# Performance work log

Hardware: AMD Instinct MI355X
Metric: run time of the kernel (lower is better)

The kernel has to match this reference:

```python
import jax, jax.numpy as jnp
import numpy as np

N = 200000
E = 3200000
EPS = 1e-5


def setup_inputs() -> dict:
    key = jax.random.key(0)
    ks = jax.random.split(key, 8)
    x = jax.random.normal(ks[0], (N, 128), dtype=jnp.float32)
    edge_index = jax.random.randint(ks[1], (2, E), 0, N, dtype=jnp.int32)
    def lin(k, fi, fo):
        s = 1.0 / np.sqrt(fi)
        return jax.random.uniform(k, (fi, fo), jnp.float32, -s, s)
    return {
        "x": x,
        "edge_index": edge_index,
        "W1": lin(ks[2], 128, 256), "b1": jnp.zeros((256,), jnp.float32),
        "gamma1": jnp.ones((256,), jnp.float32), "beta1": jnp.zeros((256,), jnp.float32),
        "W2": lin(ks[3], 256, 256), "b2": jnp.zeros((256,), jnp.float32),
        "gamma2": jnp.ones((256,), jnp.float32), "beta2": jnp.zeros((256,), jnp.float32),
        "W3": lin(ks[4], 256, 40), "b3": jnp.zeros((40,), jnp.float32),
    }


def _gcn_norm(edge_index):
    # add self-loops, compute symmetric GCN normalization
    loop = jnp.arange(N, dtype=jnp.int32)
    row = jnp.concatenate([edge_index[0], loop])
    col = jnp.concatenate([edge_index[1], loop])
    deg = jax.ops.segment_sum(jnp.ones_like(row, dtype=jnp.float32), row, num_segments=N)
    dinv = jax.lax.rsqrt(jnp.maximum(deg, 1.0))  # deg >= 1 due to self-loops
    norm = dinv[row] * dinv[col]  # [E+N]
    return row, col, norm


def _gcn_conv(x, W, b, row, col, norm):
    h = x @ W                                  # [N, Fout] small GEMM
    msg = h[col] * norm[:, None]               # gather + scale  [E+N, Fout]
    out = jax.ops.segment_sum(msg, row, num_segments=N)  # scatter-add
    return out + b


def _batchnorm(x, gamma, beta):
    mu = jnp.mean(x, axis=0)
    var = jnp.var(x, axis=0)
    return (x - mu) * jax.lax.rsqrt(var + EPS) * gamma + beta


def reference(x, edge_index, W1, b1, gamma1, beta1, W2, b2, gamma2, beta2, W3, b3):
    row, col, norm = _gcn_norm(edge_index)
    h = _gcn_conv(x, W1, b1, row, col, norm)
    h = jax.nn.relu(_batchnorm(h, gamma1, beta1))
    h = _gcn_conv(h, W2, b2, row, col, norm)
    h = jax.nn.relu(_batchnorm(h, gamma2, beta2))
    h = _gcn_conv(h, W3, b3, row, col, norm)
    return jax.nn.log_softmax(h, axis=-1)
```

## Files before the change

### kernel.cpp

```cpp
#include <hip/hip_runtime.h>
#include <hip/hip_bf16.h>

#define NNODES 200000
#define NEDGES 3200000
#define NBUCK 782
#define NEB 512
#define EPB (NEDGES / NEB)
#define EPS 1e-5f
#define AGGB_CHUNK 50000

typedef __bf16 bf16x8 __attribute__((ext_vector_type(8)));
typedef float  f32x4  __attribute__((ext_vector_type(4)));
typedef float  f32x2  __attribute__((ext_vector_type(2)));

__device__ __forceinline__ float bflo(unsigned u) { return __uint_as_float(u << 16); }
__device__ __forceinline__ float bfhi(unsigned u) { return __uint_as_float(u & 0xffff0000u); }
__device__ __forceinline__ unsigned short f2b(float f) {
    return __builtin_bit_cast(unsigned short, __float2bfloat16(f));
}
__device__ __forceinline__ unsigned pk2(float a, float b) {
    return (unsigned)f2b(a) | ((unsigned)f2b(b) << 16);
}
__device__ __forceinline__ unsigned bnrelu_pk(unsigned u, f32x2 c, f32x2 h) {
    f32x2 v = { __uint_as_float(u << 16), __uint_as_float(u & 0xffff0000u) };
    v = __builtin_elementwise_fma(v, c, h);
    const f32x2 z = {0.f, 0.f};
    v = __builtin_elementwise_max(v, z);
    return pk2(v[0], v[1]);
}

__device__ __forceinline__ void prepw_one(const float* __restrict__ W,
                                          unsigned short* __restrict__ Wswz,
                                          int K, int NOUT, int t) {
    int KSTEPS = K / 32;
    int lane = t & 63;
    int ks = (t >> 6) % KSTEPS;
    int g  = (t >> 6) / KSTEPS;
    int c = lane & 15, q = lane >> 4;
    int col = g * 16 + c;
    int k0 = ks * 32 + q * 8;
    unsigned short vals[8];
#pragma unroll
    for (int j = 0; j < 8; ++j)
        vals[j] = (col < NOUT) ? f2b(W[(size_t)(k0 + j) * NOUT + col]) : (unsigned short)0;
    *(uint4*)((char*)Wswz + (size_t)t * 16) = __builtin_bit_cast(uint4, vals);
}

__global__ __launch_bounds__(256) void k_cnt(const int* __restrict__ row, int* __restrict__ cnt,
                                             const float* __restrict__ W1,
                                             const float* __restrict__ W2,
                                             const float* __restrict__ W3,
                                             unsigned short* __restrict__ w1s,
                                             unsigned short* __restrict__ w2s,
                                             unsigned short* __restrict__ w3s,
                                             unsigned* __restrict__ statsz) {
    const int blk = blockIdx.x;
    if (blk == NEB + 54) {
        for (int i = threadIdx.x; i < 1026; i += 256) statsz[i] = 0u;
        return;
    }
    if (blk >= NEB) {
        int t = (blk - NEB) * 256 + threadIdx.x;
        if (t < 4096) prepw_one(W1, w1s, 128, 256, t);
        else if (t < 12288) prepw_one(W2, w2s, 256, 256, t - 4096);
        else if (t < 13824) prepw_one(W3, w3s, 256, 40, t - 12288);
        return;
    }
    __shared__ int h[NBUCK];
    for (int i = threadIdx.x; i < NBUCK; i += 256) h[i] = 0;
    __syncthreads();
    const int e0 = blk * EPB;
    for (int i = e0 + threadIdx.x; i < e0 + EPB; i += 256)
        atomicAdd(&h[row[i] >> 8], 1);
    __syncthreads();
    for (int i = threadIdx.x; i < NBUCK; i += 256)
        cnt[(size_t)blk * NBUCK + i] = h[i];
}

__global__ __launch_bounds__(256) void k_bscan(int* __restrict__ cnt, int* __restrict__ btot) {
    const int wv = (blockIdx.x * 256 + threadIdx.x) >> 6;
    const int lane = threadIdx.x & 63;
    if (wv >= NBUCK) return;
    int v[8]; int s = 0;
#pragma unroll
    for (int j = 0; j < 8; ++j) {
        v[j] = cnt[(size_t)(lane * 8 + j) * NBUCK + wv];
        s += v[j];
    }
    int excl = s;
#pragma unroll
    for (int o = 1; o < 64; o <<= 1) {
        int t = __shfl_up(excl, o);
        if (lane >= o) excl += t;
    }
    excl -= s;
    if (lane == 63) btot[wv] = excl + s;
    int base = excl;
#pragma unroll
    for (int j = 0; j < 8; ++j) {
        int t = v[j];
        cnt[(size_t)(lane * 8 + j) * NBUCK + wv] = base;
        base += t;
    }
}

__global__ __launch_bounds__(256) void k_place(const int* __restrict__ row, const int* __restrict__ col,
                                               const int* __restrict__ cnt, const int* __restrict__ btot,
                                               int* __restrict__ bbase, unsigned* __restrict__ ebuf) {
    __shared__ int sbb[NBUCK];
    __shared__ int tp[256];
    __shared__ int base[NBUCK];
    const int t = threadIdx.x;
    int v[4]; int loc = 0;
    const int i0 = t * 4;
#pragma unroll
    for (int j = 0; j < 4; ++j) {
        int idx = i0 + j;
        v[j] = (idx < NBUCK) ? btot[idx] : 0;
        loc += v[j];
    }
    tp[t] = loc;
    __syncthreads();
    for (int off = 1; off < 256; off <<= 1) {
        int u = (t >= off) ? tp[t - off] : 0;
        __syncthreads();
        tp[t] += u;
        __syncthreads();
    }
    int run = tp[t] - loc;
#pragma unroll
    for (int j = 0; j < 4; ++j) {
        int idx = i0 + j;
        if (idx < NBUCK) sbb[idx] = run;
        run += v[j];
    }
    __syncthreads();
    if (blockIdx.x == 0) {
        for (int i = t; i < NBUCK; i += 256) bbase[i] = sbb[i];
        if (t == 0) bbase[NBUCK] = NEDGES;
    }
    for (int i = t; i < NBUCK; i += 256)
        base[i] = sbb[i] + cnt[(size_t)blockIdx.x * NBUCK + i];
    __syncthreads();
    const int e0 = blockIdx.x * EPB;
    for (int i = e0 + t; i < e0 + EPB; i += 256) {
        int r = row[i], c = col[i];
        int p = atomicAdd(&base[r >> 8], 1);
        ebuf[p] = ((unsigned)(r & 255) << 18) | (unsigned)c;
    }
}

__global__ __launch_bounds__(256) void k_sort2(const unsigned* __restrict__ ebuf,
                                               const int* __restrict__ bbase,
                                               int* __restrict__ offs, float* __restrict__ dinv,
                                               int* __restrict__ csr,
                                               const float* __restrict__ x,
                                               uint4* __restrict__ xb) {
    __shared__ int cnt[256];
    __shared__ int sofs[256];
    __shared__ int sc[256];
    __shared__ float sdinv[256];
    const int b = blockIdx.x;
    const int t = threadIdx.x;
    const int n0 = b * 256;
    cnt[t] = 0;
    __syncthreads();
    const int s = bbase[b], e = bbase[b + 1];
    for (int i = s + t; i < e; i += 256)
        atomicAdd(&cnt[ebuf[i] >> 18], 1);
    __syncthreads();
    const int c = cnt[t];
    sc[t] = c;
    __syncthreads();
    for (int off = 1; off < 256; off <<= 1) {
        int v = (t >= off) ? sc[t - off] : 0;
        __syncthreads();
        sc[t] += v;
        __syncthreads();
    }
    const int excl = sc[t] - c;
    sofs[t] = s + excl;
    const int n = n0 + t;
    float dv = rsqrtf((float)(c + 1));
    sdinv[t] = dv;
    if (n < NNODES) {
        offs[n] = s + excl;
        dinv[n] = dv;
    }
    if (b == NBUCK - 1 && t == 0) offs[NNODES] = NEDGES;
    cnt[t] = 0;
    __syncthreads();
    for (int i = s + t; i < e; i += 256) {
        unsigned v = ebuf[i];
        int nl = v >> 18;
        int rank = atomicAdd(&cnt[nl], 1);
        csr[sofs[nl] + rank] = (int)(v & 0x3FFFFu);
    }
    const int nn = (NNODES - n0 < 256) ? (NNODES - n0) : 256;
    const float4* xp = (const float4*)(x + (size_t)n0 * 128);
    uint4* xo = xb + (size_t)n0 * 16;
    const int lim = nn * 16;
    for (int i = t; i < lim; i += 256) {
        float d = sdinv[i >> 4];
        float4 a = xp[i * 2], bb = xp[i * 2 + 1];
        uint4 o;
        o.x = pk2(a.x * d, a.y * d);  o.y = pk2(a.z * d, a.w * d);
        o.z = pk2(bb.x * d, bb.y * d); o.w = pk2(bb.z * d, bb.w * d);
        xo[i] = o;
    }
}

__global__ __launch_bounds__(256) void k_aggf(const uint4* __restrict__ in,
                                              const int* __restrict__ offs,
                                              const int* __restrict__ csr,
                                              const float* __restrict__ dinv,
                                              uint4* __restrict__ out) {
    const int lane = threadIdx.x & 63;
    const int grp = lane >> 4;
    const int fl = lane & 15;
    const int node = blockIdx.x * 4 + (threadIdx.x >> 6);
    const int p0 = offs[node];
    const int K = offs[node + 1] - p0 + 1;
    float a0=0,a1=0,a2=0,a3=0,a4=0,a5=0,a6=0,a7=0;
    auto accum = [&](uint4 u) {
        a0 += bflo(u.x); a1 += bfhi(u.x);
        a2 += bflo(u.y); a3 += bfhi(u.y);
        a4 += bflo(u.z); a5 += bfhi(u.z);
        a6 += bflo(u.w); a7 += bfhi(u.w);
    };
    int k = 0;
    for (; k + 16 <= K; k += 16) {
        int j0 = k + grp;
        int i0 = (j0 == 0) ? node : csr[p0 + j0 - 1];
        int i1 = csr[p0 + k + 3 + grp];
        int i2 = csr[p0 + k + 7 + grp];
        int i3 = csr[p0 + k + 11 + grp];
        uint4 u0 = in[(size_t)i0 * 16 + fl];
        uint4 u1 = in[(size_t)i1 * 16 + fl];
        uint4 u2 = in[(size_t)i2 * 16 + fl];
        uint4 u3 = in[(size_t)i3 * 16 + fl];
        accum(u0); accum(u1); accum(u2); accum(u3);
    }
    for (; k + 8 <= K; k += 8) {
        int j0 = k + grp;
        int i0 = (j0 == 0) ? node : csr[p0 + j0 - 1];
        int i1 = csr[p0 + k + 3 + grp];
        uint4 u0 = in[(size_t)i0 * 16 + fl];
        uint4 u1 = in[(size_t)i1 * 16 + fl];
        accum(u0); accum(u1);
    }
    for (; k + 4 <= K; k += 4) {
        int j0 = k + grp;
        int i0 = (j0 == 0) ? node : csr[p0 + j0 - 1];
        accum(in[(size_t)i0 * 16 + fl]);
    }
    int rem = K - k;
    if (grp < rem) {
        int j0 = k + grp;
        int i0 = (j0 == 0) ? node : csr[p0 + j0 - 1];
        accum(in[(size_t)i0 * 16 + fl]);
    }
#define RED(v) v += __shfl_xor(v, 32); v += __shfl_xor(v, 16);
    RED(a0) RED(a1) RED(a2) RED(a3) RED(a4) RED(a5) RED(a6) RED(a7)
#undef RED
    if (grp == 0) {
        const float d = dinv[node];
        uint4 o;
        o.x = pk2(a0 * d, a1 * d); o.y = pk2(a2 * d, a3 * d);
        o.z = pk2(a4 * d, a5 * d); o.w = pk2(a6 * d, a7 * d);
        out[(size_t)node * 16 + fl] = o;
    }
}

__global__ __launch_bounds__(256) void k_aggb(const uint4* __restrict__ in,
                                              const int* __restrict__ offs,
                                              const int* __restrict__ csr,
                                              const float* __restrict__ dinv,
                                              uint4* __restrict__ out,
                                              int nbase) {
    const int lane = threadIdx.x & 63;
    const int half = lane >> 5;
    const int fl = lane & 31;
    const int node = nbase + blockIdx.x * 4 + (threadIdx.x >> 6);
    const int p0 = offs[node];
    const int K = offs[node + 1] - p0 + 1;
    float a0=0,a1=0,a2=0,a3=0,a4=0,a5=0,a6=0,a7=0;
    auto accum = [&](uint4 u) {
        a0 += bflo(u.x); a1 += bfhi(u.x);
        a2 += bflo(u.y); a3 += bfhi(u.y);
        a4 += bflo(u.z); a5 += bfhi(u.z);
        a6 += bflo(u.w); a7 += bfhi(u.w);
    };
    auto idxAt = [&](int j) -> int { return (j == 0) ? node : csr[p0 + j - 1]; };
    int k = 0;
    for (; k + 8 <= K; k += 8) {
        int i0 = idxAt(k + half);
        int i1 = csr[p0 + k + 1 + half];
        int i2 = csr[p0 + k + 3 + half];
        int i3 = csr[p0 + k + 5 + half];
        uint4 u0 = in[(size_t)i0 * 32 + fl];
        uint4 u1 = in[(size_t)i1 * 32 + fl];
        uint4 u2 = in[(size_t)i2 * 32 + fl];
        uint4 u3 = in[(size_t)i3 * 32 + fl];
        accum(u0); accum(u1); accum(u2); accum(u3);
    }
    for (; k + 2 <= K; k += 2) {
        accum(in[(size_t)idxAt(k + half) * 32 + fl]);
    }
    if (k < K && half == 0) {
        accum(in[(size_t)idxAt(k) * 32 + fl]);
    }
#define RED(v) v += __shfl_xor(v, 32);
    RED(a0) RED(a1) RED(a2) RED(a3) RED(a4) RED(a5) RED(a6) RED(a7)
#undef RED
    if (half == 0) {
        const float d = dinv[node];
        uint4 o;
        o.x = pk2(a0 * d, a1 * d); o.y = pk2(a2 * d, a3 * d);
        o.z = pk2(a4 * d, a5 * d); o.w = pk2(a6 * d, a7 * d);
        out[(size_t)node * 32 + fl] = o;
    }
}

__global__ __launch_bounds__(256) void k_agg3(const uint4* __restrict__ T3b,
                                              const int* __restrict__ offs,
                                              const int* __restrict__ csr,
                                              const float* __restrict__ dinv,
                                              const float* __restrict__ b3,
                                              float* __restrict__ out) {
    const int lane = threadIdx.x & 63;
    const int grp = lane / 5;
    const int fl = lane - grp * 5;
    const bool act = grp < 12;
    const int node = blockIdx.x * 4 + (threadIdx.x >> 6);
    const int p0 = offs[node];
    const int K = offs[node + 1] - p0 + 1;
    float a0=0,a1=0,a2=0,a3=0,a4=0,a5=0,a6=0,a7=0;
    auto accum = [&](uint4 u) {
        a0 += bflo(u.x); a1 += bfhi(u.x);
        a2 += bflo(u.y); a3 += bfhi(u.y);
        a4 += bflo(u.z); a5 += bfhi(u.z);
        a6 += bflo(u.w); a7 += bfhi(u.w);
    };
    const char* Tb = (const char*)T3b;
    int k = 0;
    if (act) {
        for (; k + 12 <= K; k += 12) {
            int j = k + grp;
            int i0 = (j == 0) ? node : csr[p0 + j - 1];
            accum(*(const uint4*)(Tb + (size_t)i0 * 128 + fl * 16));
        }
        int rem = K - k;
        if (grp < rem) {
            int j = k + grp;
            int i0 = (j == 0) ? node : csr[p0 + j - 1];
            accum(*(const uint4*)(Tb + (size_t)i0 * 128 + fl * 16));
        }
    }
#define RED3(v) { float t = __shfl(v, lane + 30); v += t; t = __shfl(v, lane + 15); v += t; \
                  float u1 = __shfl(v, lane + 5); float u2 = __shfl(v, lane + 10); v += u1 + u2; }
    RED3(a0) RED3(a1) RED3(a2) RED3(a3) RED3(a4) RED3(a5) RED3(a6) RED3(a7)
#undef RED3
    const float d = dinv[node];
    float v[8];
    if (grp == 0) {
        const float4* bp = (const float4*)(b3 + fl * 8);
        float4 b01 = bp[0], b23 = bp[1];
        v[0] = a0 * d + b01.x; v[1] = a1 * d + b01.y;
        v[2] = a2 * d + b01.z; v[3] = a3 * d + b01.w;
        v[4] = a4 * d + b23.x; v[5] = a5 * d + b23.y;
        v[6] = a6 * d + b23.z; v[7] = a7 * d + b23.w;
    } else {
#pragma unroll
        for (int j = 0; j < 8; ++j) v[j] = -INFINITY;
    }
    float m = v[0];
#pragma unroll
    for (int j = 1; j < 8; ++j) m = fmaxf(m, v[j]);
    float mm = __shfl(m, 0);
#pragma unroll
    for (int l = 1; l < 5; ++l) mm = fmaxf(mm, __shfl(m, l));
    float e = 0.f;
    if (grp == 0) {
#pragma unroll
        for (int j = 0; j < 8; ++j) e += __expf(v[j] - mm);
    }
    float s = __shfl(e, 0);
#pragma unroll
    for (int l = 1; l < 5; ++l) s += __shfl(e, l);
    float ls = __logf(s);
    if (grp == 0) {
        float* op = out + (size_t)node * 40 + fl * 8;
        float4 o0 = {v[0] - mm - ls, v[1] - mm - ls, v[2] - mm - ls, v[3] - mm - ls};
        float4 o1 = {v[4] - mm - ls, v[5] - mm - ls, v[6] - mm - ls, v[7] - mm - ls};
        *(float4*)op = o0;
        *(float4*)(op + 4) = o1;
    }
}

template <int K, int MW, int NW, int WNB, bool PRESCALE, bool BNA, bool STATS>
__global__ __launch_bounds__(MW * NW * 64) void k_gemm(const __hip_bfloat16* __restrict__ A,
                                                       const __hip_bfloat16* __restrict__ Wswz,
                                                       const float* __restrict__ dinvp,
                                                       const float* __restrict__ bnsc,
                                                       const float* __restrict__ bnsh,
                                                       unsigned short* __restrict__ Cout,
                                                       int M, int NOUT, int CS,
                                                       float* __restrict__ sums,
                                                       float* __restrict__ sq,
                                                       const float* __restrict__ gamma,
                                                       const float* __restrict__ beta,
                                                       float* __restrict__ scale,
                                                       float* __restrict__ shift,
                                                       int* __restrict__ done) {
    constexpr int KSTEPS = K / 32;
    const int lane = threadIdx.x & 63;
    const int wid  = threadIdx.x >> 6;
    const int wm = (wid % MW) * 64;
    const int wn = (wid / MW) * (WNB * 16);
    const long rowBase = (long)blockIdx.x * (MW * 64);
    const int cl = lane & 15, q = lane >> 4;

    const __hip_bfloat16* aptr[4];
#pragma unroll
    for (int mf = 0; mf < 4; ++mf) {
        long r = rowBase + wm + mf * 16 + cl;
        if (r > M - 1) r = M - 1;
        aptr[mf] = A + r * K + q * 8;
    }
    const __hip_bfloat16* bptr[WNB];
#pragma unroll
    for (int nf = 0; nf < WNB; ++nf) {
        int g = wn / 16 + nf;
        bptr[nf] = Wswz + (size_t)g * KSTEPS * 512 + (size_t)lane * 8;
    }

    f32x4 acc[4][WNB];
    const f32x4 z = {0.f, 0.f, 0.f, 0.f};
#pragma unroll
    for (int mf = 0; mf < 4; ++mf)
#pragma unroll
        for (int nf = 0; nf < WNB; ++nf) acc[mf][nf] = z;

#pragma unroll
    for (int ks = 0; ks < KSTEPS; ++ks) {
        f32x2 cp0, cp1, cp2, cp3, hp0, hp1, hp2, hp3;
        if constexpr (BNA) {
            const int k0 = ks * 32 + q * 8;
            const f32x2* cp = (const f32x2*)(bnsc + k0);
            const f32x2* hp = (const f32x2*)(bnsh + k0);
            cp0 = cp[0]; cp1 = cp[1]; cp2 = cp[2]; cp3 = cp[3];
            hp0 = hp[0]; hp1 = hp[1]; hp2 = hp[2]; hp3 = hp[3];
        }
        bf16x8 a[4], b[WNB];
#pragma unroll
        for (int mf = 0; mf < 4; ++mf) {
            uint4 u = *(const uint4*)(aptr[mf] + ks * 32);
            if constexpr (BNA) {
                uint4 o;
                o.x = bnrelu_pk(u.x, cp0, hp0);
                o.y = bnrelu_pk(u.y, cp1, hp1);
                o.z = bnrelu_pk(u.z, cp2, hp2);
                o.w = bnrelu_pk(u.w, cp3, hp3);
                u = o;
            }
            a[mf] = __builtin_bit_cast(bf16x8, u);
        }
#pragma unroll
        for (int nf = 0; nf < WNB; ++nf)
            b[nf] = __builtin_bit_cast(bf16x8, *(const uint4*)(bptr[nf] + ks * 512));
#pragma unroll
        for (int mf = 0; mf < 4; ++mf)
#pragma unroll
            for (int nf = 0; nf < WNB; ++nf)
                acc[mf][nf] = __builtin_amdgcn_mfma_f32_16x16x32_bf16(a[mf], b[nf], acc[mf][nf], 0, 0, 0);
    }

#pragma unroll
    for (int mf = 0; mf < 4; ++mf)
#pragma unroll
        for (int i = 0; i < 4; ++i) {
            long row = rowBase + wm + mf * 16 + q * 4 + i;
            if (row >= M) continue;
            float dv = PRESCALE ? dinvp[row] : 1.0f;
#pragma unroll
            for (int nf = 0; nf < WNB; ++nf) {
                int col = wn + nf * 16 + cl;
                if (col < NOUT)
                    Cout[row * CS + col] = f2b(PRESCALE ? acc[mf][nf][i] * dv : acc[mf][nf][i]);
            }
        }

    if constexpr (STATS) {
#pragma unroll
        for (int nf = 0; nf < WNB; ++nf) {
            float s = 0.f, s2 = 0.f;
#pragma unroll
            for (int mf = 0; mf < 4; ++mf)
#pragma unroll
                for (int i = 0; i < 4; ++i) {
                    long row = rowBase + wm + mf * 16 + q * 4 + i;
                    float v = (row < M) ? acc[mf][nf][i] : 0.f;
                    s += v; s2 += v * v;
                }
            s  += __shfl_xor(s, 16);  s  += __shfl_xor(s, 32);
            s2 += __shfl_xor(s2, 16); s2 += __shfl_xor(s2, 32);
            if (q == 0) {
                int col = wn + nf * 16 + cl;
                if (col < NOUT) {
                    atomicAdd(&sums[col], s);
                    atomicAdd(&sq[col], s2);
                }
            }
        }
        __syncthreads();
        __shared__ int lastf;
        if (threadIdx.x == 0) lastf = (atomicAdd(done, 1) == (int)gridDim.x - 1) ? 1 : 0;
        __syncthreads();
        if (lastf) {
            const int tt = threadIdx.x;
            float su = atomicAdd(&sums[tt], 0.0f);
            float qu = atomicAdd(&sq[tt], 0.0f);
            float mu = su * (1.0f / NNODES);
            float var = qu * (1.0f / NNODES) - mu * mu;
            if (var < 0.f) var = 0.f;
            float sc = gamma[tt] * rsqrtf(var + EPS);
            scale[tt] = sc;
            shift[tt] = beta[tt] - mu * sc;
        }
    }
}

__global__ __launch_bounds__(256) void k_stats(const uint4* __restrict__ Zu,
                                               float* __restrict__ sums, float* __restrict__ sq,
                                               const float* __restrict__ gamma,
                                               const float* __restrict__ beta,
                                               float* __restrict__ scale, float* __restrict__ shift,
                                               int* __restrict__ done) {
    __shared__ float reds[8][256];
    __shared__ float redq[8][256];
    const int t = threadIdx.x;
    const int cg = t & 31;
    const int rs = t >> 5;
    const long r0 = (long)blockIdx.x * 256 + (long)rs * 32;
    float s[8], q[8];
#pragma unroll
    for (int j = 0; j < 8; ++j) { s[j] = 0.f; q[j] = 0.f; }
    for (int i = 0; i < 32; ++i) {
        long r = r0 + i;
        if (r >= NNODES) break;
        uint4 u = Zu[r * 32 + cg];
        float v0 = bflo(u.x), v1 = bfhi(u.x), v2 = bflo(u.y), v3 = bfhi(u.y);
        float v4 = bflo(u.z), v5 = bfhi(u.z), v6 = bflo(u.w), v7 = bfhi(u.w);
        s[0] += v0; q[0] += v0 * v0;  s[1] += v1; q[1] += v1 * v1;
        s[2] += v2; q[2] += v2 * v2;  s[3] += v3; q[3] += v3 * v3;
        s[4] += v4; q[4] += v4 * v4;  s[5] += v5; q[5] += v5 * v5;
        s[6] += v6; q[6] += v6 * v6;  s[7] += v7; q[7] += v7 * v7;
    }
#pragma unroll
    for (int j = 0; j < 8; ++j) {
        reds[rs][cg * 8 + j] = s[j];
        redq[rs][cg * 8 + j] = q[j];
    }
    __syncthreads();
    float S = 0.f, Q = 0.f;
#pragma unroll
    for (int j = 0; j < 8; ++j) { S += reds[j][t]; Q += redq[j][t]; }
    atomicAdd(&sums[t], S);
    atomicAdd(&sq[t], Q);
    __syncthreads();
    __shared__ int lastf;
    if (t == 0) lastf = (atomicAdd(done, 1) == (int)gridDim.x - 1) ? 1 : 0;
    __syncthreads();
    if (lastf) {
        float su = atomicAdd(&sums[t], 0.0f);
        float qu = atomicAdd(&sq[t], 0.0f);
        float mu = su * (1.0f / NNODES);
        float var = qu * (1.0f / NNODES) - mu * mu;
        if (var < 0.f) var = 0.f;
        float sc = gamma[t] * rsqrtf(var + EPS);
        scale[t] = sc;
        shift[t] = beta[t] - mu * sc;
    }
}

extern "C" void kernel_launch(void* const* d_in, const int* in_sizes, int n_in,
                              void* d_out, int out_size, void* d_ws, size_t ws_size,
                              hipStream_t stream) {
    const float* x   = (const float*)d_in[0];
    const int*   ei  = (const int*)d_in[1];
    const float* W1  = (const float*)d_in[2];
    const float* g1  = (const float*)d_in[4];
    const float* be1 = (const float*)d_in[5];
    const float* W2  = (const float*)d_in[6];
    const float* g2  = (const float*)d_in[8];
    const float* be2 = (const float*)d_in[9];
    const float* W3  = (const float*)d_in[10];
    const float* b3  = (const float*)d_in[11];

    char* w = (char*)d_ws;
    size_t o = 0;
    auto alloc = [&](size_t b) { size_t r = o; o += (b + 255) & ~(size_t)255; return r; };
    int*   offs = (int*)(w + alloc((size_t)(NNODES + 1) * 4));
    float* dinv = (float*)(w + alloc((size_t)NNODES * 4));
    int*   cnt  = (int*)(w + alloc((size_t)NEB * NBUCK * 4));
    int*   btot = (int*)(w + alloc(NBUCK * 4));
    int*   bbase= (int*)(w + alloc((NBUCK + 1) * 4));
    unsigned* ebuf = (unsigned*)(w + alloc((size_t)NEDGES * 4));
    int*   csr  = (int*)(w + alloc((size_t)NEDGES * 4));
    float* stats = (float*)(w + alloc(4 * 256 * 4 + 32));
    float* bnp   = (float*)(w + alloc(4 * 256 * 4));
    unsigned short* w1s = (unsigned short*)(w + alloc(65536));
    unsigned short* w2s = (unsigned short*)(w + alloc(131072));
    unsigned short* w3s = (unsigned short*)(w + alloc(24576));
    __hip_bfloat16* xb   = (__hip_bfloat16*)(w + alloc((size_t)NNODES * 128 * 2));
    __hip_bfloat16* buf0 = (__hip_bfloat16*)(w + alloc((size_t)NNODES * 128 * 2));
    __hip_bfloat16* buf1 = (__hip_bfloat16*)(w + alloc((size_t)NNODES * 256 * 2));
    __hip_bfloat16* buf2 = (__hip_bfloat16*)(w + alloc((size_t)NNODES * 256 * 2));

    float* sums1 = stats;       float* sq1 = stats + 256;
    float* sums2 = stats + 512; float* sq2 = stats + 768;
    int*   done1 = (int*)(stats + 1024);
    int*   done2 = done1 + 1;
    float* scale1 = bnp;        float* shift1 = bnp + 256;
    float* scale2 = bnp + 512;  float* shift2 = bnp + 768;

    const int SB = (NNODES + 255) / 256;

    k_cnt<<<NEB + 55, 256, 0, stream>>>(ei, cnt, W1, W2, W3, w1s, w2s, w3s, (unsigned*)stats);
    k_bscan<<<(NBUCK * 64 + 255) / 256, 256, 0, stream>>>(cnt, btot);
    k_place<<<NEB, 256, 0, stream>>>(ei, ei + NEDGES, cnt, btot, bbase, ebuf);
    k_sort2<<<NBUCK, 256, 0, stream>>>(ebuf, bbase, offs, dinv, csr, x, (uint4*)xb);

    const dim3 g64((NNODES + 63) / 64, 1);

    k_aggf<<<NNODES / 4, 256, 0, stream>>>((const uint4*)xb, offs, csr, dinv, (uint4*)buf0);
    k_gemm<128, 1, 4, 4, false, false, true><<<g64, 256, 0, stream>>>(buf0, (const __hip_bfloat16*)w1s, nullptr, nullptr, nullptr, (unsigned short*)buf1, NNODES, 256, 256, sums1, sq1, g1, be1, scale1, shift1, done1);

    k_gemm<256, 1, 4, 4, true, true, false><<<g64, 256, 0, stream>>>(buf1, (const __hip_bfloat16*)w2s, dinv, scale1, shift1, (unsigned short*)buf2, NNODES, 256, 256, nullptr, nullptr, nullptr, nullptr, nullptr, nullptr, nullptr);
    for (int c = 0; c < 4; ++c)
        k_aggb<<<AGGB_CHUNK / 4, 256, 0, stream>>>((const uint4*)buf2, offs, csr, dinv, (uint4*)buf1, c * AGGB_CHUNK);
    k_stats<<<SB, 256, 0, stream>>>((const uint4*)buf1, sums2, sq2, g2, be2, scale2, shift2, done2);

    k_gemm<256, 4, 1, 3, true, true, false><<<dim3((NNODES + 255) / 256, 1), 256, 0, stream>>>(buf1, (const __hip_bfloat16*)w3s, dinv, scale2, shift2, (unsigned short*)buf0, NNODES, 40, 64, nullptr, nullptr, nullptr, nullptr, nullptr, nullptr, nullptr);
    k_agg3<<<NNODES / 4, 256, 0, stream>>>((const uint4*)buf0, offs, csr, dinv, b3, (float*)d_out);
}
```

Baseline: 1.094 ms.

## Stage A tiles through double-buffered LDS with register prefetch in GEMM

The GEMM's A operand was loaded straight from global memory into MFMA registers per wave, and each wave redundantly applied the BN+ReLU transform. Now the whole block cooperatively loads each K-step tile into registers, applies BN+ReLU once, stores it to a double-buffered shared-memory tile, and prefetches the next step while MFMAs run. The aim is to remove redundant global loads across waves sharing rows and to overlap memory latency with compute. The cost is extra LDS traffic, a barrier per K-step and possible LDS bank conflicts from the 64-byte row stride.

```diff
diff --git a/kernel.cpp b/kernel.cpp
--- a/kernel.cpp
+++ b/kernel.cpp
@@ -414,20 +414,20 @@
                                                        float* __restrict__ shift,
                                                        int* __restrict__ done) {
     constexpr int KSTEPS = K / 32;
-    const int lane = threadIdx.x & 63;
-    const int wid  = threadIdx.x >> 6;
+    constexpr int NTHR   = MW * NW * 64;
+    constexpr int ROWS   = MW * 64;
+    constexpr int STAGE_U4 = (ROWS * 64) / (NTHR * 16);
+    __shared__ __align__(16) unsigned short As[2][ROWS * 32];
+
+    const int t = threadIdx.x;
+    const int lane = t & 63;
+    const int wid  = t >> 6;
     const int wm = (wid % MW) * 64;
     const int wn = (wid / MW) * (WNB * 16);
-    const long rowBase = (long)blockIdx.x * (MW * 64);
+    const long rowBase = (long)blockIdx.x * ROWS;
     const int cl = lane & 15, q = lane >> 4;
-
-    const __hip_bfloat16* aptr[4];
-#pragma unroll
-    for (int mf = 0; mf < 4; ++mf) {
-        long r = rowBase + wm + mf * 16 + cl;
-        if (r > M - 1) r = M - 1;
-        aptr[mf] = A + r * K + q * 8;
-    }
+    const int colq = t & 3;
+
     const __hip_bfloat16* bptr[WNB];
 #pragma unroll
     for (int nf = 0; nf < WNB; ++nf) {
@@ -435,6 +435,37 @@
         bptr[nf] = Wswz + (size_t)g * KSTEPS * 512 + (size_t)lane * 8;
     }
 
+    uint4 stg[STAGE_U4];
+    auto stage_ld = [&](int ks) {
+#pragma unroll
+        for (int u = 0; u < STAGE_U4; ++u) {
+            int rg = (t >> 2) + u * (NTHR >> 2);
+            long r = rowBase + rg; if (r > M - 1) r = M - 1;
+            stg[u] = *(const uint4*)((const char*)A + (size_t)r * (K * 2) + ks * 64 + colq * 16);
+        }
+    };
+    auto stage_st = [&](int ks, int bsel) {
+        f32x2 cp[4], hp[4];
+        if constexpr (BNA) {
+            const f32x2* cpp = (const f32x2*)(bnsc + ks * 32 + colq * 8);
+            const f32x2* hpp = (const f32x2*)(bnsh + ks * 32 + colq * 8);
+#pragma unroll
+            for (int j = 0; j < 4; ++j) { cp[j] = cpp[j]; hp[j] = hpp[j]; }
+        }
+#pragma unroll
+        for (int u = 0; u < STAGE_U4; ++u) {
+            uint4 v = stg[u];
+            if constexpr (BNA) {
+                v.x = bnrelu_pk(v.x, cp[0], hp[0]);
+                v.y = bnrelu_pk(v.y, cp[1], hp[1]);
+                v.z = bnrelu_pk(v.z, cp[2], hp[2]);
+                v.w = bnrelu_pk(v.w, cp[3], hp[3]);
+            }
+            int rg = (t >> 2) + u * (NTHR >> 2);
+            *(uint4*)&As[bsel][rg * 32 + colq * 8] = v;
+        }
+    };
+
     f32x4 acc[4][WNB];
     const f32x4 z = {0.f, 0.f, 0.f, 0.f};
 #pragma unroll
@@ -442,38 +473,30 @@
 #pragma unroll
         for (int nf = 0; nf < WNB; ++nf) acc[mf][nf] = z;
 
+    stage_ld(0);
+    stage_st(0, 0);
+    __syncthreads();
+
 #pragma unroll
     for (int ks = 0; ks < KSTEPS; ++ks) {
-        f32x2 cp0, cp1, cp2, cp3, hp0, hp1, hp2, hp3;
-        if constexpr (BNA) {
-            const int k0 = ks * 32 + q * 8;
-            const f32x2* cp = (const f32x2*)(bnsc + k0);
-            const f32x2* hp = (const f32x2*)(bnsh + k0);
-            cp0 = cp[0]; cp1 = cp[1]; cp2 = cp[2]; cp3 = cp[3];
-            hp0 = hp[0]; hp1 = hp[1]; hp2 = hp[2]; hp3 = hp[3];
-        }
+        const int cur = ks & 1;
+        if (ks + 1 < KSTEPS) stage_ld(ks + 1);
         bf16x8 a[4], b[WNB];
-#pragma unroll
-        for (int mf = 0; mf < 4; ++mf) {
-            uint4 u = *(const uint4*)(aptr[mf] + ks * 32);
-            if constexpr (BNA) {
-                uint4 o;
-                o.x = bnrelu_pk(u.x, cp0, hp0);
-                o.y = bnrelu_pk(u.y, cp1, hp1);
-                o.z = bnrelu_pk(u.z, cp2, hp2);
-                o.w = bnrelu_pk(u.w, cp3, hp3);
-                u = o;
-            }
-            a[mf] = __builtin_bit_cast(bf16x8, u);
-        }
 #pragma unroll
         for (int nf = 0; nf < WNB; ++nf)
             b[nf] = __builtin_bit_cast(bf16x8, *(const uint4*)(bptr[nf] + ks * 512));
 #pragma unroll
         for (int mf = 0; mf < 4; ++mf)
+            a[mf] = __builtin_bit_cast(bf16x8, *(const uint4*)&As[cur][(wm + mf * 16 + cl) * 32 + q * 8]);
+#pragma unroll
+        for (int mf = 0; mf < 4; ++mf)
 #pragma unroll
             for (int nf = 0; nf < WNB; ++nf)
                 acc[mf][nf] = __builtin_amdgcn_mfma_f32_16x16x32_bf16(a[mf], b[nf], acc[mf][nf], 0, 0, 0);
+        if (ks + 1 < KSTEPS) {
+            stage_st(ks + 1, cur ^ 1);
+            __syncthreads();
+        }
     }
 
 #pragma unroll
```

New measurement: 1.035 ms. 1.06x faster.
